# Kernel tuning notes

Measured on AMD Instinct MI355X. Metric: run time of the kernel, lower is better.

## Reference

```python
import jax, jax.numpy as jnp
import numpy as np
import math

B, T, D = 4, 4096, 1024
N, L = 256, 768
H = 16
TE = 1024  # time_embed_dim


def _ln(x, g, b, eps=1e-5):
    mu = jnp.mean(x, axis=-1, keepdims=True)
    var = jnp.var(x, axis=-1, keepdims=True)
    return (x - mu) * jax.lax.rsqrt(var + eps) * g + b


def setup_inputs() -> dict:
    key = jax.random.key(0)
    ks = jax.random.split(key, 12)
    s = lambda fan_in: 1.0 / math.sqrt(fan_in)
    return {
        "x":   jax.random.normal(ks[0], (B, T, D), jnp.float32),
        "xf":  jax.random.normal(ks[1], (B, N, L), jnp.float32),
        "emb": jax.random.normal(ks[2], (B, TE), jnp.float32),
        # LayerNorm params
        "norm_g": jnp.ones((D,), jnp.float32), "norm_b": jnp.zeros((D,), jnp.float32),
        "tnorm_g": jnp.ones((L,), jnp.float32), "tnorm_b": jnp.zeros((L,), jnp.float32),
        # Q/K/V projections
        "Wq": jax.random.uniform(ks[3], (D, D), jnp.float32, -s(D), s(D)),
        "bq": jnp.zeros((D,), jnp.float32),
        "Wk": jax.random.uniform(ks[4], (L, D), jnp.float32, -s(L), s(L)),
        "bk": jnp.zeros((D,), jnp.float32),
        "Wv": jax.random.uniform(ks[5], (L, D), jnp.float32, -s(L), s(L)),
        "bv": jnp.zeros((D,), jnp.float32),
        # StylizationBlock: emb_layers Linear(TE, 2D)
        "We": jax.random.uniform(ks[6], (TE, 2 * D), jnp.float32, -s(TE), s(TE)),
        "be": jnp.zeros((2 * D,), jnp.float32),
        # StylizationBlock: inner LayerNorm + out Linear(D, D)
        "snorm_g": jnp.ones((D,), jnp.float32), "snorm_b": jnp.zeros((D,), jnp.float32),
        "Wo": jax.random.uniform(ks[7], (D, D), jnp.float32, -s(D), s(D)),
        "bo": jnp.zeros((D,), jnp.float32),
    }


def reference(x, xf, emb, norm_g, norm_b, tnorm_g, tnorm_b,
              Wq, bq, Wk, bk, Wv, bv, We, be, snorm_g, snorm_b, Wo, bo):
    dh = D // H
    xf_n = _ln(xf, tnorm_g, tnorm_b)                      # B,N,L (shared by K and V)
    q = (_ln(x, norm_g, norm_b) @ Wq + bq).reshape(B, T, H, dh)
    k = (xf_n @ Wk + bk).reshape(B, N, H, dh)
    v = (xf_n @ Wv + bv).reshape(B, N, H, dh)
    attn = jnp.einsum('bthd,bnhd->btnh', q, k) / math.sqrt(dh)
    w = jax.nn.softmax(attn, axis=2)                      # softmax over text tokens n
    y = jnp.einsum('btnh,bnhd->bthd', w, v).reshape(B, T, D)
    # StylizationBlock (AdaLN-style)
    emb_out = jax.nn.silu(emb) @ We + be                  # B, 2D
    scale, shift = jnp.split(emb_out[:, None, :], 2, axis=2)
    h = _ln(y, snorm_g, snorm_b) * (1.0 + scale) + shift
    h = jax.nn.silu(h) @ Wo + bo
    return x + h
```

## Files before the change

### kernel.cpp

```cpp
#include <hip/hip_runtime.h>

typedef unsigned short u16;
typedef short bf16x8 __attribute__((ext_vector_type(8)));
typedef float f32x4 __attribute__((ext_vector_type(4)));


__device__ __forceinline__ float b2f(u16 u) {
  union { unsigned int u; float f; } x; x.u = ((unsigned int)u) << 16; return x.f;
}
__device__ __forceinline__ u16 f2b(float f) {
  union { float f; unsigned int u; } x; x.f = f;
  unsigned int u = x.u;
  return (u16)((u + 0x7FFFu + ((u >> 16) & 1u)) >> 16);
}

#define GLOAD_LDS16(g, l)                                                      \
  __builtin_amdgcn_global_load_lds(                                            \
      (const __attribute__((address_space(1))) unsigned int*)(g),              \
      (__attribute__((address_space(3))) unsigned int*)(l), 16, 0, 0)

__global__ __launch_bounds__(256) void transpose4_k(
    const float* __restrict__ Wq, const float* __restrict__ Wk,
    const float* __restrict__ Wv, const float* __restrict__ Wo,
    u16* __restrict__ wqt, u16* __restrict__ wkt,
    u16* __restrict__ wvt, u16* __restrict__ wot,
    float* __restrict__ embo) {
  if (blockIdx.z == 0 && blockIdx.y == 0) {
    int idx = blockIdx.x * 256 + threadIdx.y * 32 + threadIdx.x;
    embo[idx] = 0.f;
  }
  const float* src; u16* dst; int R;
  switch (blockIdx.z) {
    case 0: src = Wq; dst = wqt; R = 1024; break;
    case 1: src = Wk; dst = wkt; R = 768;  break;
    case 2: src = Wv; dst = wvt; R = 768;  break;
    default: src = Wo; dst = wot; R = 1024; break;
  }
  int bx = blockIdx.x * 32, by = blockIdx.y * 32;
  if (by >= R) return;
  __shared__ float t[32][33];
  int x = threadIdx.x, y = threadIdx.y;
#pragma unroll
  for (int i = 0; i < 4; ++i)
    t[y * 4 + i][x] = src[(size_t)(by + y * 4 + i) * 1024 + bx + x];
  __syncthreads();
#pragma unroll
  for (int i = 0; i < 4; ++i)
    dst[(size_t)(bx + y * 4 + i) * R + by + x] = f2b(t[x][y * 4 + i]);
}

__global__ __launch_bounds__(256) void ln_k(const float* __restrict__ in,
                                            const float* __restrict__ g,
                                            const float* __restrict__ bta,
                                            u16* __restrict__ out, int C) {
  int row = blockIdx.x, tid = threadIdx.x;
  const float* p = in + (size_t)row * C;
  int i0 = tid * 4;
  bool act = i0 < C;
  float v0 = 0.f, v1 = 0.f, v2 = 0.f, v3 = 0.f;
  if (act) {
    float4 u = *(const float4*)(p + i0);
    v0 = u.x; v1 = u.y; v2 = u.z; v3 = u.w;
  }
  float s = v0 + v1 + v2 + v3;
  float q = v0 * v0 + v1 * v1 + v2 * v2 + v3 * v3;
  __shared__ float red[8];
#pragma unroll
  for (int m = 32; m; m >>= 1) { s += __shfl_xor(s, m); q += __shfl_xor(q, m); }
  if ((tid & 63) == 0) { red[tid >> 6] = s; red[4 + (tid >> 6)] = q; }
  __syncthreads();
  s = red[0] + red[1] + red[2] + red[3];
  q = red[4] + red[5] + red[6] + red[7];
  float invC = 1.0f / (float)C;
  float mu = s * invC;
  float rs = rsqrtf(q * invC - mu * mu + 1e-5f);
  if (act) {
    float4 ug = *(const float4*)(g + i0);
    float4 ub = *(const float4*)(bta + i0);
    ushort4 o;
    o.x = f2b((v0 - mu) * rs * ug.x + ub.x);
    o.y = f2b((v1 - mu) * rs * ug.y + ub.y);
    o.z = f2b((v2 - mu) * rs * ug.z + ub.z);
    o.w = f2b((v3 - mu) * rs * ug.w + ub.w);
    *(ushort4*)(out + (size_t)row * C + i0) = o;
  }
}

__global__ __launch_bounds__(256) void style_k(const u16* __restrict__ y,
                                               const float* __restrict__ g,
                                               const float* __restrict__ bta,
                                               const float* __restrict__ embo,
                                               u16* __restrict__ out) {
  int row = blockIdx.x, tid = threadIdx.x;
  int b = row >> 12;
  const u16* p = y + (size_t)row * 1024;
  int i0 = tid * 4;
  ushort4 u = *(const ushort4*)(p + i0);
  float v0 = b2f(u.x), v1 = b2f(u.y), v2 = b2f(u.z), v3 = b2f(u.w);
  float s = v0 + v1 + v2 + v3;
  float q = v0 * v0 + v1 * v1 + v2 * v2 + v3 * v3;
  __shared__ float red[8];
#pragma unroll
  for (int m = 32; m; m >>= 1) { s += __shfl_xor(s, m); q += __shfl_xor(q, m); }
  if ((tid & 63) == 0) { red[tid >> 6] = s; red[4 + (tid >> 6)] = q; }
  __syncthreads();
  s = red[0] + red[1] + red[2] + red[3];
  q = red[4] + red[5] + red[6] + red[7];
  const float invC = 1.0f / 1024.0f;
  float mu = s * invC;
  float rs = rsqrtf(q * invC - mu * mu + 1e-5f);
  float4 ug = *(const float4*)(g + i0);
  float4 ub = *(const float4*)(bta + i0);
  float4 sc = *(const float4*)(embo + b * 2048 + i0);
  float4 sh = *(const float4*)(embo + b * 2048 + 1024 + i0);
  float h0 = ((v0 - mu) * rs * ug.x + ub.x) * (1.0f + sc.x) + sh.x;
  float h1 = ((v1 - mu) * rs * ug.y + ub.y) * (1.0f + sc.y) + sh.y;
  float h2 = ((v2 - mu) * rs * ug.z + ub.z) * (1.0f + sc.z) + sh.z;
  float h3 = ((v3 - mu) * rs * ug.w + ub.w) * (1.0f + sc.w) + sh.w;
  ushort4 o;
  o.x = f2b(h0 / (1.0f + __expf(-h0)));
  o.y = f2b(h1 / (1.0f + __expf(-h1)));
  o.z = f2b(h2 / (1.0f + __expf(-h2)));
  o.w = f2b(h3 / (1.0f + __expf(-h3)));
  *(ushort4*)(out + (size_t)row * 1024 + i0) = o;
}

__global__ __launch_bounds__(256) void emb_k(const float* __restrict__ emb,
                                             const float* __restrict__ We,
                                             const float* __restrict__ be,
                                             float* __restrict__ embo) {
  int b = blockIdx.y, tid = threadIdx.x;
  int j = blockIdx.x * 256 + tid;
  int i0 = blockIdx.z * 128;
  __shared__ float se[128];
  if (tid < 128) {
    float v = emb[b * 1024 + i0 + tid];
    se[tid] = v / (1.0f + __expf(-v));
  }
  __syncthreads();
  float acc = (blockIdx.z == 0) ? be[j] : 0.f;
#pragma unroll 8
  for (int i = 0; i < 128; ++i) acc += se[i] * We[(size_t)(i0 + i) * 2048 + j];
  atomicAdd(&embo[b * 2048 + j], acc);
}

__global__ __launch_bounds__(256) void kvproj_k(const u16* __restrict__ A,
                                                const u16* __restrict__ WkT,
                                                const u16* __restrict__ WvT,
                                                const float* __restrict__ bk_,
                                                const float* __restrict__ bv_,
                                                u16* __restrict__ Ck,
                                                u16* __restrict__ Cv) {
  const int K = 768, Nn = 1024;
  const u16* Bt = blockIdx.z ? WvT : WkT;
  const float* bias = blockIdx.z ? bv_ : bk_;
  __shared__ __align__(16) short As[128 * 64];
  __shared__ __align__(16) short Bs[128 * 64];
  int tid = threadIdx.x;
  int m0 = blockIdx.x * 128, n0 = blockIdx.y * 128;
  int wave = tid >> 6, lane = tid & 63;
  int l16 = lane & 15, quad = lane >> 4;
  int wm = (wave >> 1) * 64, wn = (wave & 1) * 64;

  f32x4 acc[4][4];
#pragma unroll
  for (int i = 0; i < 4; ++i)
#pragma unroll
    for (int j = 0; j < 4; ++j)
#pragma unroll
      for (int r = 0; r < 4; ++r) acc[i][j][r] = 0.f;

  for (int kt = 0; kt < K; kt += 64) {
#pragma unroll
    for (int p = 0; p < 4; ++p) {
      int c = p * 256 + tid;
      int r = c >> 3;
      int cd = ((c & 7) ^ (r & 7)) * 8;
      int lb = (p * 256 + wave * 64) * 8;
      GLOAD_LDS16(A + (size_t)(m0 + r) * K + kt + cd, As + lb);
      GLOAD_LDS16(Bt + (size_t)(n0 + r) * K + kt + cd, Bs + lb);
    }
    __syncthreads();
#pragma unroll
    for (int ks = 0; ks < 2; ++ks) {
      int swz = ((ks * 4 + quad) ^ (l16 & 7)) * 8;
      bf16x8 af[4], bfr[4];
#pragma unroll
      for (int i = 0; i < 4; ++i)
        af[i] = *(const bf16x8*)&As[(wm + i * 16 + l16) * 64 + swz];
#pragma unroll
      for (int j = 0; j < 4; ++j)
        bfr[j] = *(const bf16x8*)&Bs[(wn + j * 16 + l16) * 64 + swz];
#pragma unroll
      for (int i = 0; i < 4; ++i)
#pragma unroll
        for (int j = 0; j < 4; ++j)
          acc[i][j] = __builtin_amdgcn_mfma_f32_16x16x32_bf16(af[i], bfr[j], acc[i][j], 0, 0, 0);
    }
    __syncthreads();
  }

#pragma unroll
  for (int j = 0; j < 4; ++j) {
    int col = n0 + wn + j * 16 + l16;
    float bv = bias[col];
#pragma unroll
    for (int i = 0; i < 4; ++i) {
      int row0 = m0 + wm + i * 16 + quad * 4;
#pragma unroll
      for (int r = 0; r < 4; ++r) {
        int row = row0 + r;
        float v = acc[i][j][r] + bv;
        if (blockIdx.z) {
          Cv[((size_t)((row >> 8) * 1024 + col)) * 256 + (row & 255)] = f2b(v);
        } else {
          Ck[(size_t)row * Nn + col] = f2b(v);
        }
      }
    }
  }
}

__global__ __launch_bounds__(512, 4) void gemm256_k(const u16* __restrict__ A,
                                                    const u16* __restrict__ Bt,
                                                    const float* __restrict__ bias,
                                                    const float* __restrict__ res,
                                                    u16* __restrict__ Cb,
                                                    float* __restrict__ Cf,
                                                    int M, int Nn, int K, int mode) {
  __shared__ __align__(16) short smem[36864];
  short* AsB = smem;
  short* BsB = smem + 12288;
  int tid = threadIdx.x;
  int m0 = blockIdx.x * 128, n0 = blockIdx.y * 256;
  int wave = tid >> 6, lane = tid & 63;
  int l16 = lane & 15, quad = lane >> 4;
  int wm = (wave >> 2) * 64;
  int wn = (wave & 3) * 64;

  size_t offA;
  {
    int r = tid >> 2;
    int cg = (tid & 3) ^ ((r >> 1) & 3);
    offA = (size_t)(m0 + r) * K + cg * 8;
  }
  int ldsA = tid * 8;
  size_t offB[2];
  int ldsB[2];
#pragma unroll
  for (int p = 0; p < 2; ++p) {
    int c = p * 512 + tid;
    int r = c >> 2;
    int cg = (c & 3) ^ ((r >> 1) & 3);
    offB[p] = (size_t)(n0 + r) * K + cg * 8;
    ldsB[p] = c * 8;
  }

  int aoff[4], boff[4];
#pragma unroll
  for (int mi = 0; mi < 4; ++mi) {
    int R = wm + mi * 16 + l16;
    aoff[mi] = R * 32 + ((quad ^ ((R >> 1) & 3)) * 8);
  }
#pragma unroll
  for (int ni = 0; ni < 4; ++ni) {
    int R = wn + ni * 16 + l16;
    boff[ni] = R * 32 + ((quad ^ ((R >> 1) & 3)) * 8);
  }

  f32x4 acc[4][4];
#pragma unroll
  for (int i = 0; i < 4; ++i)
#pragma unroll
    for (int j = 0; j < 4; ++j)
#pragma unroll
      for (int r = 0; r < 4; ++r) acc[i][j][r] = 0.f;

#define STAGE(tt, bufc)                                                        \
  do {                                                                         \
    int kt_ = (tt) * 32;                                                       \
    GLOAD_LDS16(A + offA + kt_, AsB + (bufc) * 4096 + ldsA);                   \
    GLOAD_LDS16(Bt + offB[0] + kt_, BsB + (bufc) * 8192 + ldsB[0]);            \
    GLOAD_LDS16(Bt + offB[1] + kt_, BsB + (bufc) * 8192 + ldsB[1]);            \
  } while (0)

#define COMPUTE(curc)                                                          \
  do {                                                                         \
    const short* as_ = AsB + (curc) * 4096;                                    \
    const short* bs_ = BsB + (curc) * 8192;                                    \
    bf16x8 af[4], bfv[4];                                                      \
    _Pragma("unroll") for (int mi = 0; mi < 4; ++mi)                           \
        af[mi] = *(const bf16x8*)&as_[aoff[mi]];                               \
    _Pragma("unroll") for (int ni = 0; ni < 4; ++ni)                           \
        bfv[ni] = *(const bf16x8*)&bs_[boff[ni]];                              \
    __builtin_amdgcn_s_setprio(1);                                             \
    _Pragma("unroll") for (int mi = 0; mi < 4; ++mi)                           \
      _Pragma("unroll") for (int ni = 0; ni < 4; ++ni)                         \
        acc[mi][ni] = __builtin_amdgcn_mfma_f32_16x16x32_bf16(                 \
            af[mi], bfv[ni], acc[mi][ni], 0, 0, 0);                            \
    __builtin_amdgcn_s_setprio(0);                                             \
  } while (0)

  const int NT = K >> 5;
  STAGE(0, 0);
  STAGE(1, 1);

  int cur = 0;
  for (int t = 0; t < NT - 1; ++t) {
    asm volatile("s_waitcnt vmcnt(3)" ::: "memory");
    __builtin_amdgcn_s_barrier();
    asm volatile("" ::: "memory");
    if (t + 2 < NT) {
      int nb = cur + 2; if (nb >= 3) nb -= 3;
      STAGE(t + 2, nb);
    }
    COMPUTE(cur);
    cur = (cur == 2) ? 0 : cur + 1;
  }
  asm volatile("s_waitcnt vmcnt(0)" ::: "memory");
  __builtin_amdgcn_s_barrier();
  asm volatile("" ::: "memory");
  COMPUTE(cur);
#undef COMPUTE
#undef STAGE

  float* eps = (float*)smem;
  float bv[4];
#pragma unroll
  for (int ni = 0; ni < 4; ++ni) bv[ni] = bias[n0 + wn + ni * 16 + l16];

#pragma unroll
  for (int half = 0; half < 2; ++half) {
    __syncthreads();
    if ((wave >> 2) == half) {
#pragma unroll
      for (int mi = 0; mi < 4; ++mi) {
#pragma unroll
        for (int ni = 0; ni < 4; ++ni) {
          int col = wn + ni * 16 + l16;
#pragma unroll
          for (int r = 0; r < 4; ++r) {
            int row = mi * 16 + quad * 4 + r;
            eps[row * 256 + (col ^ (((row >> 2) & 3) << 3))] =
                acc[mi][ni][r] + bv[ni];
          }
        }
      }
    }
    __syncthreads();
#pragma unroll
    for (int p = 0; p < 8; ++p) {
      int row = wave * 8 + p;
      int grow = m0 + half * 64 + row;
      int colb = (lane * 4) ^ (((row >> 2) & 3) << 3);
      f32x4 v = *(const f32x4*)&eps[row * 256 + colb];
      if (mode == 2) {
        float4 rv = ((const float4*)&res[(size_t)grow * Nn + n0])[lane];
        float4 o;
        o.x = v[0] + rv.x; o.y = v[1] + rv.y;
        o.z = v[2] + rv.z; o.w = v[3] + rv.w;
        ((float4*)&Cf[(size_t)grow * Nn + n0])[lane] = o;
      } else {
        ushort4 o;
        o.x = f2b(v[0]); o.y = f2b(v[1]); o.z = f2b(v[2]); o.w = f2b(v[3]);
        ((ushort4*)&Cb[(size_t)grow * Nn + n0])[lane] = o;
      }
    }
  }
}

__global__ __launch_bounds__(256) void attn_k(const u16* __restrict__ Q,
                                              const u16* __restrict__ Kt,
                                              const u16* __restrict__ VT,
                                              u16* __restrict__ Y) {
  __shared__ __align__(16) short KsPs[256 * 64];
  int tid = threadIdx.x;
  int t0 = blockIdx.x * 64, h = blockIdx.y, b = blockIdx.z;
  int wave = tid >> 6, lane = tid & 63;
  int l16 = lane & 15, quad = lane >> 4;
  int wb = wave * 16;

#pragma unroll
  for (int p = 0; p < 8; ++p) {
    int c = p * 256 + tid;
    int n = c >> 3, s = c & 7;
    GLOAD_LDS16(Kt + ((size_t)(b * 256 + n)) * 1024 + h * 64 + ((s ^ (n & 7)) * 8),
                KsPs + (p * 256 + wave * 64) * 8);
  }
  const u16* qrow = Q + ((size_t)(b * 4096 + t0 + wb + l16)) * 1024 + h * 64;
  bf16x8 qf0 = *(const bf16x8*)(qrow + quad * 8);
  bf16x8 qf1 = *(const bf16x8*)(qrow + 32 + quad * 8);
  asm volatile("s_waitcnt vmcnt(0)" ::: "memory");
  __syncthreads();

  f32x4 sa[16];
#pragma unroll
  for (int mt = 0; mt < 16; ++mt)
#pragma unroll
    for (int r = 0; r < 4; ++r) sa[mt][r] = 0.f;
#pragma unroll
  for (int ks = 0; ks < 2; ++ks) {
    bf16x8 qb = ks ? qf1 : qf0;
#pragma unroll
    for (int mt = 0; mt < 16; ++mt) {
      int n = mt * 16 + l16;
      bf16x8 kf = *(const bf16x8*)&KsPs[n * 64 + (((ks * 4 + quad) ^ (n & 7)) * 8)];
      sa[mt] = __builtin_amdgcn_mfma_f32_16x16x32_bf16(kf, qb, sa[mt], 0, 0, 0);
    }
  }
  __syncthreads();

  const float CLG = 0.18033688011112042f;
  float mx = -3.0e38f;
#pragma unroll
  for (int mt = 0; mt < 16; ++mt)
#pragma unroll
    for (int r = 0; r < 4; ++r) mx = fmaxf(mx, sa[mt][r]);
  mx = fmaxf(mx, __shfl_xor(mx, 16));
  mx = fmaxf(mx, __shfl_xor(mx, 32));
  float mxc = mx * CLG;
  float sum = 0.f;
#pragma unroll
  for (int mt = 0; mt < 16; ++mt)
#pragma unroll
    for (int r = 0; r < 4; ++r) {
      float e = __builtin_exp2f(sa[mt][r] * CLG - mxc);
      sa[mt][r] = e;
      sum += e;
    }
  sum += __shfl_xor(sum, 16);
  sum += __shfl_xor(sum, 32);
  float rsc = 1.0f / sum;

  {
    int prow = wb + l16;
    short* pb = &KsPs[prow * 256 + (quad & 1) * 4];
    int q2 = quad >> 1, swz = l16 & 7;
#pragma unroll
    for (int mt = 0; mt < 16; ++mt) {
      float a0 = sa[mt][0], a1 = sa[mt][1], a2 = sa[mt][2], a3 = sa[mt][3];
      unsigned plo, phi;
      asm("v_cvt_pk_bf16_f32 %0, %1, %2" : "=v"(plo) : "v"(a0), "v"(a1));
      asm("v_cvt_pk_bf16_f32 %0, %1, %2" : "=v"(phi) : "v"(a2), "v"(a3));
      uint2 pk; pk.x = plo; pk.y = phi;
      *(uint2*)(pb + (((2 * mt + q2) ^ swz) * 8)) = pk;
    }
  }
  __syncthreads();

  const u16* vb = VT + ((size_t)(b * 1024 + h * 64)) * 256;
  f32x4 ya[4];
#pragma unroll
  for (int j = 0; j < 4; ++j)
#pragma unroll
    for (int r = 0; r < 4; ++r) ya[j][r] = 0.f;
  int m = wb + l16;
#pragma unroll
  for (int kk = 0; kk < 8; ++kk) {
    bf16x8 af = *(const bf16x8*)&KsPs[m * 256 + (((kk * 4 + quad) ^ (m & 7)) * 8)];
#pragma unroll
    for (int j = 0; j < 4; ++j) {
      bf16x8 bfr = *(const bf16x8*)(vb + (size_t)(j * 16 + l16) * 256 + kk * 32 + quad * 8);
      ya[j] = __builtin_amdgcn_mfma_f32_16x16x32_bf16(af, bfr, ya[j], 0, 0, 0);
    }
  }
  float rscv[4];
#pragma unroll
  for (int r = 0; r < 4; ++r) rscv[r] = __shfl(rsc, quad * 4 + r);
#pragma unroll
  for (int j = 0; j < 4; ++j)
#pragma unroll
    for (int r = 0; r < 4; ++r)
      Y[((size_t)(b * 4096 + t0 + wb + quad * 4 + r)) * 1024 + h * 64 + j * 16 + l16] =
          f2b(ya[j][r] * rscv[r]);
}

extern "C" void kernel_launch(void* const* d_in, const int* in_sizes, int n_in,
                              void* d_out, int out_size, void* d_ws, size_t ws_size,
                              hipStream_t stream) {
  const float* x       = (const float*)d_in[0];
  const float* xf      = (const float*)d_in[1];
  const float* emb     = (const float*)d_in[2];
  const float* norm_g  = (const float*)d_in[3];
  const float* norm_b  = (const float*)d_in[4];
  const float* tnorm_g = (const float*)d_in[5];
  const float* tnorm_b = (const float*)d_in[6];
  const float* Wq      = (const float*)d_in[7];
  const float* bq      = (const float*)d_in[8];
  const float* Wk      = (const float*)d_in[9];
  const float* bk      = (const float*)d_in[10];
  const float* Wv      = (const float*)d_in[11];
  const float* bv      = (const float*)d_in[12];
  const float* We      = (const float*)d_in[13];
  const float* be      = (const float*)d_in[14];
  const float* snorm_g = (const float*)d_in[15];
  const float* snorm_b = (const float*)d_in[16];
  const float* Wo      = (const float*)d_in[17];
  const float* bo      = (const float*)d_in[18];

  const size_t MB = 1024 * 1024;
  char* dout = (char*)d_out;
  u16* qbuf = (u16*)(dout);
  u16* wqt  = (u16*)(dout + 32 * MB);
  u16* wkt  = (u16*)(dout + 34 * MB);
  u16* wvt  = (u16*)(dout + 36 * MB);
  float* out = (float*)d_out;

  char* ws = (char*)d_ws;
  u16* big1 = (u16*)(ws);
  u16* xfn  = (u16*)(ws + 32 * MB);
  u16* kws  = (u16*)(ws + 33 * MB + 512 * 1024);
  u16* vtws = (u16*)(ws + 35 * MB + 512 * 1024);
  u16* wot  = (u16*)(ws + 37 * MB + 512 * 1024);
  float* embo = (float*)(ws + 39 * MB + 512 * 1024);

  transpose4_k<<<dim3(32, 32, 4), dim3(32, 8), 0, stream>>>(
      Wq, Wk, Wv, Wo, wqt, wkt, wvt, wot, embo);

  ln_k<<<16384, 256, 0, stream>>>(x, norm_g, norm_b, big1, 1024);
  ln_k<<<1024, 256, 0, stream>>>(xf, tnorm_g, tnorm_b, xfn, 768);

  gemm256_k<<<dim3(128, 4), 512, 0, stream>>>(big1, wqt, bq, nullptr, qbuf, nullptr, 16384, 1024, 1024, 0);
  kvproj_k<<<dim3(8, 8, 2), 256, 0, stream>>>(xfn, wkt, wvt, bk, bv, kws, vtws);

  emb_k<<<dim3(8, 4, 8), 256, 0, stream>>>(emb, We, be, embo);

  attn_k<<<dim3(64, 16, 4), 256, 0, stream>>>(qbuf, kws, vtws, big1);

  style_k<<<16384, 256, 0, stream>>>(big1, snorm_g, snorm_b, embo, big1);

  gemm256_k<<<dim3(128, 4), 512, 0, stream>>>(big1, wot, bo, x, nullptr, out, 16384, 1024, 1024, 2);
}
```

Before: 386.8 us.

## Use head-major Q/Y layout, stage V in LDS, fuse text LayerNorm into transpose

Q projection output and attention output now use a head-major [b,h,t,64] layout, so attention reads Q rows and writes Y rows contiguously. Y is staged through LDS to produce 16-byte coalesced stores. V^T is loaded into LDS with a swizzle instead of being read from global memory inside the MFMA loop. The text LayerNorm is folded into the weight-transpose launch as an extra z-slice, removing one kernel launch. In exchange attention uses more LDS, which may lower occupancy, and style_k now gathers each row from strided head chunks; attention writes Y in place over qbuf.

Result: faster. 361.7 us (-6.5%).

```diff
diff --git a/kernel.cpp b/kernel.cpp
--- a/kernel.cpp
+++ b/kernel.cpp
@@ -24,7 +24,44 @@
     const float* __restrict__ Wv, const float* __restrict__ Wo,
     u16* __restrict__ wqt, u16* __restrict__ wkt,
     u16* __restrict__ wvt, u16* __restrict__ wot,
-    float* __restrict__ embo) {
+    float* __restrict__ embo,
+    const float* __restrict__ xf, const float* __restrict__ tg,
+    const float* __restrict__ tb, u16* __restrict__ xfn) {
+  if (blockIdx.z == 4) {
+    int row = blockIdx.y * 32 + blockIdx.x;
+    int tid = threadIdx.y * 32 + threadIdx.x;
+    const float* p = xf + (size_t)row * 768;
+    int i0 = tid * 4;
+    bool act = i0 < 768;
+    float v0 = 0.f, v1 = 0.f, v2 = 0.f, v3 = 0.f;
+    if (act) {
+      float4 u = *(const float4*)(p + i0);
+      v0 = u.x; v1 = u.y; v2 = u.z; v3 = u.w;
+    }
+    float s = v0 + v1 + v2 + v3;
+    float q = v0 * v0 + v1 * v1 + v2 * v2 + v3 * v3;
+    __shared__ float red[8];
+#pragma unroll
+    for (int m = 32; m; m >>= 1) { s += __shfl_xor(s, m); q += __shfl_xor(q, m); }
+    if ((tid & 63) == 0) { red[tid >> 6] = s; red[4 + (tid >> 6)] = q; }
+    __syncthreads();
+    s = red[0] + red[1] + red[2] + red[3];
+    q = red[4] + red[5] + red[6] + red[7];
+    const float invC = 1.0f / 768.0f;
+    float mu = s * invC;
+    float rs = rsqrtf(q * invC - mu * mu + 1e-5f);
+    if (act) {
+      float4 ug = *(const float4*)(tg + i0);
+      float4 ub = *(const float4*)(tb + i0);
+      ushort4 o;
+      o.x = f2b((v0 - mu) * rs * ug.x + ub.x);
+      o.y = f2b((v1 - mu) * rs * ug.y + ub.y);
+      o.z = f2b((v2 - mu) * rs * ug.z + ub.z);
+      o.w = f2b((v3 - mu) * rs * ug.w + ub.w);
+      *(ushort4*)(xfn + (size_t)row * 768 + i0) = o;
+    }
+    return;
+  }
   if (blockIdx.z == 0 && blockIdx.y == 0) {
     int idx = blockIdx.x * 256 + threadIdx.y * 32 + threadIdx.x;
     embo[idx] = 0.f;
@@ -93,9 +130,10 @@
                                                u16* __restrict__ out) {
   int row = blockIdx.x, tid = threadIdx.x;
   int b = row >> 12;
-  const u16* p = y + (size_t)row * 1024;
+  int t = row & 4095;
   int i0 = tid * 4;
-  ushort4 u = *(const ushort4*)(p + i0);
+  int h = i0 >> 6, c = i0 & 63;
+  ushort4 u = *(const ushort4*)(y + ((size_t)((b * 16 + h) * 4096 + t)) * 64 + c);
   float v0 = b2f(u.x), v1 = b2f(u.y), v2 = b2f(u.z), v3 = b2f(u.w);
   float s = v0 + v1 + v2 + v3;
   float q = v0 * v0 + v1 * v1 + v2 * v2 + v3 * v3;
@@ -363,7 +401,14 @@
       } else {
         ushort4 o;
         o.x = f2b(v[0]); o.y = f2b(v[1]); o.z = f2b(v[2]); o.w = f2b(v[3]);
-        ((ushort4*)&Cb[(size_t)grow * Nn + n0])[lane] = o;
+        if (mode == 3) {
+          int col0 = n0 + lane * 4;
+          int hh = col0 >> 6, cc = col0 & 63;
+          int bb = grow >> 12, tt = grow & 4095;
+          *(ushort4*)(Cb + ((size_t)((bb * 16 + hh) * 4096 + tt)) * 64 + cc) = o;
+        } else {
+          ((ushort4*)&Cb[(size_t)grow * Nn + n0])[lane] = o;
+        }
       }
     }
   }
@@ -374,6 +419,7 @@
                                               const u16* __restrict__ VT,
                                               u16* __restrict__ Y) {
   __shared__ __align__(16) short KsPs[256 * 64];
+  __shared__ __align__(16) short Vt[64 * 256];
   int tid = threadIdx.x;
   int t0 = blockIdx.x * 64, h = blockIdx.y, b = blockIdx.z;
   int wave = tid >> 6, lane = tid & 63;
@@ -387,7 +433,14 @@
     GLOAD_LDS16(Kt + ((size_t)(b * 256 + n)) * 1024 + h * 64 + ((s ^ (n & 7)) * 8),
                 KsPs + (p * 256 + wave * 64) * 8);
   }
-  const u16* qrow = Q + ((size_t)(b * 4096 + t0 + wb + l16)) * 1024 + h * 64;
+#pragma unroll
+  for (int p = 0; p < 8; ++p) {
+    int c = p * 256 + tid;
+    int d = c >> 5, ch = c & 31;
+    GLOAD_LDS16(VT + ((size_t)(b * 1024 + h * 64 + d)) * 256 + ((ch ^ (d & 7)) * 8),
+                Vt + (p * 256 + wave * 64) * 8);
+  }
+  const u16* qrow = Q + ((size_t)((b * 16 + h) * 4096 + t0 + wb + l16)) * 64;
   bf16x8 qf0 = *(const bf16x8*)(qrow + quad * 8);
   bf16x8 qf1 = *(const bf16x8*)(qrow + 32 + quad * 8);
   asm volatile("s_waitcnt vmcnt(0)" ::: "memory");
@@ -448,7 +501,6 @@
   }
   __syncthreads();
 
-  const u16* vb = VT + ((size_t)(b * 1024 + h * 64)) * 256;
   f32x4 ya[4];
 #pragma unroll
   for (int j = 0; j < 4; ++j)
@@ -460,19 +512,35 @@
     bf16x8 af = *(const bf16x8*)&KsPs[m * 256 + (((kk * 4 + quad) ^ (m & 7)) * 8)];
 #pragma unroll
     for (int j = 0; j < 4; ++j) {
-      bf16x8 bfr = *(const bf16x8*)(vb + (size_t)(j * 16 + l16) * 256 + kk * 32 + quad * 8);
+      int d = j * 16 + l16;
+      bf16x8 bfr = *(const bf16x8*)&Vt[d * 256 + (((kk * 4 + quad) ^ (d & 7)) * 8)];
       ya[j] = __builtin_amdgcn_mfma_f32_16x16x32_bf16(af, bfr, ya[j], 0, 0, 0);
     }
   }
   float rscv[4];
 #pragma unroll
   for (int r = 0; r < 4; ++r) rscv[r] = __shfl(rsc, quad * 4 + r);
+
 #pragma unroll
   for (int j = 0; j < 4; ++j)
 #pragma unroll
-    for (int r = 0; r < 4; ++r)
-      Y[((size_t)(b * 4096 + t0 + wb + quad * 4 + r)) * 1024 + h * 64 + j * 16 + l16] =
-          f2b(ya[j][r] * rscv[r]);
+    for (int r = 0; r < 4; ++r) {
+      int lr = quad * 4 + r;
+      int col = j * 16 + l16;
+      int g = (col >> 3) ^ quad;
+      KsPs[(wb + lr) * 256 + g * 8 + (col & 7)] = (short)f2b(ya[j][r] * rscv[r]);
+    }
+  {
+    int lr2 = lane >> 2;
+    int sw = (lr2 >> 2) & 3;
+    int g0 = (lane & 3) * 2;
+    const short* yr = &KsPs[(wb + lr2) * 256];
+    bf16x8 y0 = *(const bf16x8*)&yr[(g0 ^ sw) * 8];
+    bf16x8 y1 = *(const bf16x8*)&yr[((g0 + 1) ^ sw) * 8];
+    u16* yg = Y + ((size_t)((b * 16 + h) * 4096 + t0 + wb + lr2)) * 64 + (lane & 3) * 16;
+    *(bf16x8*)yg = y0;
+    *(bf16x8*)(yg + 8) = y1;
+  }
 }
 
 extern "C" void kernel_launch(void* const* d_in, const int* in_sizes, int n_in,
@@ -514,20 +582,19 @@
   u16* wot  = (u16*)(ws + 37 * MB + 512 * 1024);
   float* embo = (float*)(ws + 39 * MB + 512 * 1024);
 
-  transpose4_k<<<dim3(32, 32, 4), dim3(32, 8), 0, stream>>>(
-      Wq, Wk, Wv, Wo, wqt, wkt, wvt, wot, embo);
+  transpose4_k<<<dim3(32, 32, 5), dim3(32, 8), 0, stream>>>(
+      Wq, Wk, Wv, Wo, wqt, wkt, wvt, wot, embo, xf, tnorm_g, tnorm_b, xfn);
 
   ln_k<<<16384, 256, 0, stream>>>(x, norm_g, norm_b, big1, 1024);
-  ln_k<<<1024, 256, 0, stream>>>(xf, tnorm_g, tnorm_b, xfn, 768);
-
-  gemm256_k<<<dim3(128, 4), 512, 0, stream>>>(big1, wqt, bq, nullptr, qbuf, nullptr, 16384, 1024, 1024, 0);
+
+  gemm256_k<<<dim3(128, 4), 512, 0, stream>>>(big1, wqt, bq, nullptr, qbuf, nullptr, 16384, 1024, 1024, 3);
   kvproj_k<<<dim3(8, 8, 2), 256, 0, stream>>>(xfn, wkt, wvt, bk, bv, kws, vtws);
 
   emb_k<<<dim3(8, 4, 8), 256, 0, stream>>>(emb, We, be, embo);
 
-  attn_k<<<dim3(64, 16, 4), 256, 0, stream>>>(qbuf, kws, vtws, big1);
-
-  style_k<<<16384, 256, 0, stream>>>(big1, snorm_g, snorm_b, embo, big1);
+  attn_k<<<dim3(64, 16, 4), 256, 0, stream>>>(qbuf, kws, vtws, qbuf);
+
+  style_k<<<16384, 256, 0, stream>>>(qbuf, snorm_g, snorm_b, embo, big1);
 
   gemm256_k<<<dim3(128, 4), 512, 0, stream>>>(big1, wot, bo, x, nullptr, out, 16384, 1024, 1024, 2);
 }
```
